# Optimization experiments

Hardware: AMD Instinct MI355X
Metric: run time of the kernel (lower is better)

Reference implementation:

```python
import jax, jax.numpy as jnp
from jax import lax
import numpy as np

B, IMG_H, IMG_W = 8, 256, 512
NUM_CLASSES, P = 20, 32
SCALE, TOPK, IOU_THR = 32.0, 100, 0.5


def conv2d(x, w, b, stride=1, pad=1):
    y = lax.conv_general_dilated(x, w, (stride, stride), [(pad, pad), (pad, pad)],
                                 dimension_numbers=('NCHW', 'OIHW', 'NCHW'))
    return y + b[None, :, None, None]


def bilinear_resize(img, out_h, out_w):
    # img: [..., H, W]; torch F.interpolate(mode='bilinear', align_corners=False)
    H, W = img.shape[-2], img.shape[-1]
    def idx_w(n_in, n_out):
        src = (jnp.arange(n_out, dtype=jnp.float32) + 0.5) * (n_in / n_out) - 0.5
        src = jnp.clip(src, 0.0, n_in - 1)
        i0 = jnp.floor(src).astype(jnp.int32)
        i1 = jnp.minimum(i0 + 1, n_in - 1)
        return i0, i1, src - i0.astype(jnp.float32)
    y0, y1, wy = idx_w(H, out_h)
    x0, x1, wx = idx_w(W, out_w)
    top = img[..., y0, :] * (1.0 - wy)[:, None] + img[..., y1, :] * wy[:, None]
    return top[..., x0] * (1.0 - wx) + top[..., x1] * wx


def generate_anchors(fh, fw):
    ys = (jnp.arange(fh, dtype=jnp.float32) + 0.5) * (IMG_H / fh)
    xs = (jnp.arange(fw, dtype=jnp.float32) + 0.5) * (IMG_W / fw)
    cy, cx = jnp.meshgrid(ys, xs, indexing='ij')
    h = SCALE / 2
    return jnp.stack([cx - h, cy - h, cx + h, cy + h], -1).reshape(-1, 4)


def delta_to_boxes(anchors, deltas):
    a_c = (anchors[:, :2] + anchors[:, 2:]) / 2
    a_wh = anchors[:, 2:] - anchors[:, :2]
    pc = a_c + deltas[..., :2] * a_wh
    pwh = a_wh * jnp.exp(deltas[..., 2:])
    return jnp.concatenate([pc - pwh / 2, pc + pwh / 2], -1)


def nms_single(boxes, scores, labels):
    # torchvision batched_nms: offset boxes per label, greedy NMS, return kept idxs
    N = boxes.shape[0]
    off = labels.astype(boxes.dtype) * (jnp.max(boxes) + 1.0)
    b = boxes + off[:, None]
    order = jnp.argsort(-scores)
    bs = b[order]
    area = (bs[:, 2] - bs[:, 0]) * (bs[:, 3] - bs[:, 1])
    lt = jnp.maximum(bs[:, None, :2], bs[None, :, :2])
    rb = jnp.minimum(bs[:, None, 2:], bs[None, :, 2:])
    wh = jnp.clip(rb - lt, 0.0)
    inter = wh[..., 0] * wh[..., 1]
    iou = inter / (area[:, None] + area[None, :] - inter + 1e-9)
    idxs = jnp.arange(N)
    def body(i, suppressed):
        keep_i = jnp.logical_not(suppressed[i])
        row = (iou[i] > IOU_THR) & (idxs > i)
        return jnp.where(keep_i, suppressed | row, suppressed)
    suppressed = lax.fori_loop(0, N, body, jnp.zeros(N, bool))
    keep_mask = ~suppressed
    rank = jnp.cumsum(keep_mask) - 1
    slots = jnp.where(keep_mask & (rank < TOPK), rank, TOPK)
    out = jnp.full(TOPK + 1, -1, jnp.int32).at[slots].set(order.astype(jnp.int32))
    return out[:TOPK]


def setup_inputs():
    key = jax.random.key(0)
    ks = jax.random.split(key, 17)
    def cw(k, o, i, kh, kw_):
        return jax.random.normal(k, (o, i, kh, kw_), jnp.float32) / np.sqrt(i * kh * kw_)
    return {
        'images': jax.random.normal(ks[0], (B, 3, IMG_H, IMG_W), jnp.float32),
        'w1': cw(ks[1], 64, 3, 3, 3),   'b1': jnp.zeros(64, jnp.float32),
        'w2': cw(ks[2], 128, 64, 3, 3), 'b2': jnp.zeros(128, jnp.float32),
        'w3': cw(ks[3], 256, 128, 3, 3),'b3': jnp.zeros(256, jnp.float32),
        'pw1': cw(ks[4], 256, 256, 3, 3), 'pb1': jnp.zeros(256, jnp.float32),
        'pw2': cw(ks[5], P, 256, 1, 1),   'pb2': jnp.zeros(P, jnp.float32),
        'cw_': cw(ks[6], NUM_CLASSES + 1, 256, 3, 3), 'cb': jnp.zeros(NUM_CLASSES + 1, jnp.float32),
        'bw': cw(ks[7], 4, 256, 3, 3),  'bb': jnp.zeros(4, jnp.float32),
        'kw': cw(ks[8], P, 256, 3, 3),  'kb': jnp.zeros(P, jnp.float32),
    }


def reference(images, w1, b1, w2, b2, w3, b3, pw1, pb1, pw2, pb2, cw_, cb, bw, bb, kw, kb):
    x = jax.nn.relu(conv2d(images, w1, b1, stride=2))
    x = jax.nn.relu(conv2d(x, w2, b2, stride=2))
    feat = jax.nn.relu(conv2d(x, w3, b3, stride=2))          # [B,256,32,64]
    proto = conv2d(jax.nn.relu(conv2d(feat, pw1, pb1)), pw2, pb2, pad=0)  # [B,P,32,64]
    fh, fw = feat.shape[2], feat.shape[3]
    def head(w, b, c):
        return conv2d(feat, w, b).transpose(0, 2, 3, 1).reshape(B, -1, c)
    cls = head(cw_, cb, NUM_CLASSES + 1)     # [B,N,C+1]
    box = head(bw, bb, 4)                    # [B,N,4]
    coef = head(kw, kb, P)                   # [B,N,P]
    anchors = generate_anchors(fh, fw)       # [N,4]
    probs = jax.nn.softmax(cls, -1)[..., :-1]
    scores = probs.max(-1)
    labels = probs.argmax(-1).astype(jnp.int32)
    boxes = delta_to_boxes(anchors, box)     # [B,N,4]
    keep = jax.vmap(nms_single)(boxes, scores, labels)   # [B,100], -1 pad
    valid = keep >= 0
    ki = jnp.clip(keep, 0)
    take = lambda a: jnp.take_along_axis(a, ki[..., None] if a.ndim == 3 else ki, axis=1)
    boxes_k = take(boxes) * valid[..., None]
    scores_k = take(scores) * valid
    labels_k = jnp.where(valid, take(labels), 0)
    coef_k = jnp.take_along_axis(coef, ki[..., None], axis=1)   # [B,100,P]
    m = jax.nn.sigmoid(jnp.einsum('bkp,bphw->bkhw', coef_k, proto))
    masks = bilinear_resize(m, IMG_H, IMG_W) > 0.5
    masks = masks & valid[..., None, None]
    return boxes_k, scores_k, labels_k, masks, valid
```

## Files before the change

kernel.cpp:

```cpp
#include <hip/hip_runtime.h>
#include <hip/hip_bf16.h>
#include <math.h>

#define BB 8
#define NCLS 21
#define NANCH 2048
#define TOPK_N 100

static const size_t OFF_X1HI = 0;
static const size_t OFF_X1LO = 34344960;
static const size_t OFF_X2HI = 68689920;
static const size_t OFF_X2LO = 86261760;
static const size_t OFF_FTHI = 103833600;
static const size_t OFF_FTLO = 113025024;
static const size_t ZERO_BYTES = 122216448;
static const size_t OFF_WT1  = 122216448;
static const size_t OFF_A2H  = 122223616;
static const size_t OFF_A2L  = 122371072;
static const size_t OFF_A3H  = 122518528;
static const size_t OFF_A3L  = 123108352;
static const size_t OFF_AHH  = 123698176;
static const size_t OFF_AHL  = 123993088;
static const size_t OFF_AP1H = 124288000;
static const size_t OFF_AP1L = 125467648;
static const size_t OFF_WTP2 = 126647296;
static const size_t OFF_BH   = 126680064;
static const size_t OFF_HOUT = 126680576;
static const size_t OFF_P1   = 130874880;
static const size_t OFF_PROTO= 147652096;
static const size_t OFF_BOXES= 149749248;
static const size_t OFF_SCORES=150011392;
static const size_t OFF_LABELS=150076928;
static const size_t OFF_ORDER= 150142464;
static const size_t OFF_SB   = 150208000;
static const size_t OFF_IOU  = 150470144;
static const size_t OFF_KEEP = 154664448;
static const size_t OFF_MAXB = 154668032;
static const size_t OFF_M    = 154668544;

static const size_t OUT_BOXES  = 0;
static const size_t OUT_SCORES = 3200;
static const size_t OUT_LABELS = 4000;
static const size_t OUT_MASKS  = 4800;
static const size_t OUT_VALID  = 104862400;

typedef __attribute__((ext_vector_type(8))) short bf16x8;
typedef __attribute__((ext_vector_type(4))) float f32x4;

__device__ __forceinline__ unsigned encf(float f){
  unsigned u = __float_as_uint(f);
  return (u & 0x80000000u) ? ~u : (u | 0x80000000u);
}
__device__ __forceinline__ float decf(unsigned u){
  unsigned b = (u & 0x80000000u) ? (u & 0x7fffffffu) : ~u;
  return __uint_as_float(b);
}
__device__ __forceinline__ short f2bf(float f){
  __hip_bfloat16 h = __float2bfloat16(f);
  return *(short*)&h;
}
__device__ __forceinline__ float bf2f(short h){
  return __uint_as_float(((unsigned)(unsigned short)h) << 16);
}

__global__ void initk(unsigned* maxb){
  if (threadIdx.x < BB) maxb[threadIdx.x] = 0u;
}

__global__ void zerok(float4* __restrict__ p, long n4){
  long i = (long)blockIdx.x*256 + threadIdx.x;
  if (i < n4) p[i] = make_float4(0.f,0.f,0.f,0.f);
}

template<int CIN,int COUT,int KK>
__global__ void packw(const float* __restrict__ w, float* __restrict__ wT){
  int i = blockIdx.x*256 + threadIdx.x;
  if (i >= CIN*KK*COUT) return;
  int co = i % COUT; int r = i / COUT;
  int ci = r / KK,  k = r % KK;
  wT[i] = w[(co*CIN + ci)*KK + k];
}

template<int CIN,int COUT>
__global__ void packA(const float* __restrict__ w, short* __restrict__ Ahi,
                      short* __restrict__ Alo){
  constexpr int K = CIN*9;
  constexpr int KS = K/32;
  int i = blockIdx.x*256 + threadIdx.x;
  if (i >= COUT*K) return;
  int sub  = i & 7;
  int lane = (i >> 3) & 63;
  int rest = i >> 9;
  int ks = rest % KS;
  int mt = rest / KS;
  int m = mt*16 + (lane & 15);
  int k = ks*32 + (lane >> 4)*8 + sub;
  int tap = k / CIN, ci = k - tap*CIN;
  float v = w[(m*CIN + ci)*9 + tap];
  short h = f2bf(v);
  Ahi[i] = h;
  Alo[i] = f2bf(v - bf2f(h));
}

__global__ void packAh(const float* __restrict__ cw, const float* __restrict__ bw,
                       const float* __restrict__ kw, const float* __restrict__ cb,
                       const float* __restrict__ bb, const float* __restrict__ kb,
                       short* __restrict__ Ahi, short* __restrict__ Alo,
                       float* __restrict__ bh){
  int i = blockIdx.x*256 + threadIdx.x;
  if (i < 64){
    float v = 0.f;
    if (i < 21) v = cb[i]; else if (i < 25) v = bb[i-21]; else if (i < 57) v = kb[i-25];
    bh[i] = v;
  }
  if (i >= 64*2304) return;
  constexpr int KS = 72;
  int sub  = i & 7;
  int lane = (i >> 3) & 63;
  int rest = i >> 9;
  int ks = rest % KS;
  int mt = rest / KS;
  int m = mt*16 + (lane & 15);
  int k = ks*32 + (lane >> 4)*8 + sub;
  int tap = k >> 8, ci = k & 255;
  float v = 0.f;
  if (m < 21)      v = cw[(m*256 + ci)*9 + tap];
  else if (m < 25) v = bw[((m-21)*256 + ci)*9 + tap];
  else if (m < 57) v = kw[((m-25)*256 + ci)*9 + tap];
  short h = f2bf(v);
  Ahi[i] = h;
  Alo[i] = f2bf(v - bf2f(h));
}

__global__ __launch_bounds__(256) void conv1k(const float* __restrict__ img,
    const float* __restrict__ wT, const float* __restrict__ bias,
    short* __restrict__ x1hi, short* __restrict__ x1lo){
  const int b   = blockIdx.z;
  const int co0 = blockIdx.y * 16;
  const int g   = blockIdx.x*256 + threadIdx.x;
  const int y  = g >> 7;
  const int x0 = (g & 127) << 1;

  float acc[16][2];
#pragma unroll
  for (int c=0;c<16;c++){
    float bv = bias[co0+c];
    acc[c][0] = bv; acc[c][1] = bv;
  }
  int   off[3][5];
  float msk[3][5];
#pragma unroll
  for (int kh=0;kh<3;kh++){
    int iy = y*2 - 1 + kh;
    bool okr = (iy >= 0) && (iy < 256);
    int ro = okr ? iy*512 : 0;
#pragma unroll
    for (int t=0;t<5;t++){
      int col = x0*2 - 1 + t;
      bool ok = okr && (col >= 0) && (col < 512);
      off[kh][t] = ok ? (ro + col) : 0;
      msk[kh][t] = ok ? 1.f : 0.f;
    }
  }
  const float* inb = img + (size_t)b*3*256*512;
  for (int ci=0; ci<3; ci++){
    const float* inc = inb + (size_t)ci*256*512;
    float v[3][5];
#pragma unroll
    for (int kh=0;kh<3;kh++)
#pragma unroll
      for (int t=0;t<5;t++)
        v[kh][t] = inc[off[kh][t]] * msk[kh][t];
    const float* wp = wT + ci*9*64 + co0;
#pragma unroll
    for (int kh=0;kh<3;kh++)
#pragma unroll
    for (int kw=0;kw<3;kw++){
      const float* wq = wp + (kh*3+kw)*64;
#pragma unroll
      for (int c=0;c<16;c++){
        float wv = wq[c];
        acc[c][0] = fmaf(wv, v[kh][2*0+kw], acc[c][0]);
        acc[c][1] = fmaf(wv, v[kh][2*1+kw], acc[c][1]);
      }
    }
  }
#pragma unroll
  for (int s=0;s<2;s++){
    short hv[16] __attribute__((aligned(16)));
    short lv[16] __attribute__((aligned(16)));
#pragma unroll
    for (int c=0;c<16;c++){
      float r = fmaxf(acc[c][s], 0.f);
      short h = f2bf(r);
      hv[c] = h;
      lv[c] = f2bf(r - bf2f(h));
    }
#pragma unroll
    for (int g2=0; g2<2; g2++){
      size_t ad = (((size_t)(b*8 + (co0>>3) + g2)*130 + (y+1))*258 + (x0+s+1))*8;
      *(bf16x8*)(x1hi + ad) = *(bf16x8*)(hv + g2*8);
      *(bf16x8*)(x1lo + ad) = *(bf16x8*)(lv + g2*8);
    }
  }
}

template<int CIN,int K,int M,int MW,int NW,int OW,int OHh,int S,int IPH,int IPW,
         bool SPLIT,int EMODE,int OPH,int OPW>
__global__ __launch_bounds__(NW*64) void cgemm(
    const short* __restrict__ Ahi, const short* __restrict__ Alo,
    const short* __restrict__ Bhi, const short* __restrict__ Blo,
    const float* __restrict__ bias, float* __restrict__ outf,
    short* __restrict__ outhi, short* __restrict__ outlo){
  static_assert(CIN % 32 == 0, "CIN must be multiple of 32");
  constexpr int NT = OW*OHh;
  constexpr int KS = K/32;
  constexpr int CG = CIN/8;
  const int b    = blockIdx.z;
  const int wave = threadIdx.x >> 6;
  const int lane = threadIdx.x & 63;
  const int lm = lane & 15, lq = lane >> 4;
  const int m0 = (blockIdx.y * NW + wave) * (MW*16);
  const int n0 = blockIdx.x * 64;

  int oy[4], ox[4];
#pragma unroll
  for (int j=0;j<4;j++){
    int n = n0 + j*16 + lm;
    oy[j] = n / OW; ox[j] = n % OW;
  }

  f32x4 acc[MW][4];
#pragma unroll
  for (int i=0;i<MW;i++)
#pragma unroll
    for (int j=0;j<4;j++) acc[i][j] = (f32x4){0.f,0.f,0.f,0.f};

  const short* Ah_l = Ahi + (size_t)lane*8;
  const short* Al_l = Alo + (size_t)lane*8;
  const int mt0 = m0 >> 4;

  const size_t plane = (size_t)IPH*IPW;
  const short* Bh0 = Bhi + ((size_t)b*CG + lq)*plane*8;
  const short* Bl0 = Blo + ((size_t)b*CG + lq)*plane*8;

#pragma unroll 3
  for (int tap=0; tap<9; tap++){
    const int dy = tap/3, dx = tap%3;
    size_t pix[4];
#pragma unroll
    for (int j=0;j<4;j++)
      pix[j] = (size_t)(oy[j]*S + dy)*IPW + (size_t)(ox[j]*S + dx);
    const int ksb = tap*(CIN/32);
#pragma unroll
    for (int kc=0; kc<CIN; kc+=32){
      const int ks = ksb + (kc>>5);
      const size_t koff = (size_t)(kc>>3)*plane;
      bf16x8 ah[MW], bh_[4];
#pragma unroll
      for (int i=0;i<MW;i++)
        ah[i] = *(const bf16x8*)(Ah_l + ((size_t)(mt0+i)*KS + ks)*512);
#pragma unroll
      for (int j=0;j<4;j++) bh_[j] = *(const bf16x8*)(Bh0 + (koff + pix[j])*8);
      if constexpr (SPLIT){
        bf16x8 al[MW], bl_[4];
#pragma unroll
        for (int i=0;i<MW;i++)
          al[i] = *(const bf16x8*)(Al_l + ((size_t)(mt0+i)*KS + ks)*512);
#pragma unroll
        for (int j=0;j<4;j++) bl_[j] = *(const bf16x8*)(Bl0 + (koff + pix[j])*8);
#pragma unroll
        for (int j=0;j<4;j++)
#pragma unroll
          for (int i=0;i<MW;i++)
            acc[i][j] = __builtin_amdgcn_mfma_f32_16x16x32_bf16(ah[i], bh_[j], acc[i][j], 0,0,0);
#pragma unroll
        for (int j=0;j<4;j++)
#pragma unroll
          for (int i=0;i<MW;i++)
            acc[i][j] = __builtin_amdgcn_mfma_f32_16x16x32_bf16(ah[i], bl_[j], acc[i][j], 0,0,0);
#pragma unroll
        for (int j=0;j<4;j++)
#pragma unroll
          for (int i=0;i<MW;i++)
            acc[i][j] = __builtin_amdgcn_mfma_f32_16x16x32_bf16(al[i], bh_[j], acc[i][j], 0,0,0);
      } else {
#pragma unroll
        for (int j=0;j<4;j++)
#pragma unroll
          for (int i=0;i<MW;i++)
            acc[i][j] = __builtin_amdgcn_mfma_f32_16x16x32_bf16(ah[i], bh_[j], acc[i][j], 0,0,0);
      }
    }
  }

#pragma unroll
  for (int i=0;i<MW;i++){
#pragma unroll
    for (int r=0;r<4;r++){
      const int m = m0 + i*16 + lq*4 + r;
      const float bv = bias[m];
      if constexpr (EMODE == 0){
#pragma unroll
        for (int j=0;j<4;j++){
          float v = fmaxf(acc[i][j][r] + bv, 0.f);
          short h = f2bf(v);
          short l = f2bf(v - bf2f(h));
          size_t ad = ((((size_t)(b*(M/8) + (m>>3))*OPH + (oy[j]+1))*OPW + (ox[j]+1)))*8 + (m&7);
          outhi[ad] = h;
          outlo[ad] = l;
        }
      } else {
        float* cp = outf + ((size_t)b*M + m)*NT + n0 + lm;
#pragma unroll
        for (int j=0;j<4;j++){
          float v = acc[i][j][r] + bv;
          if constexpr (EMODE == 2) v = fmaxf(v, 0.f);
          cp[j*16] = v;
        }
      }
    }
  }
}

__global__ __launch_bounds__(256) void pw2k2(const float* __restrict__ p1,
    const float* __restrict__ wT, const float* __restrict__ bias,
    float* __restrict__ proto){
  const int b  = blockIdx.y;
  const int sp = blockIdx.x*256 + threadIdx.x;
  float acc[32];
#pragma unroll
  for (int c=0;c<32;c++) acc[c] = bias[c];
  const float* pb = p1 + (size_t)b*256*NANCH + sp;
  for (int ci=0;ci<256;ci++){
    float v = pb[(size_t)ci*NANCH];
    const float* wq = wT + ci*32;
#pragma unroll
    for (int c=0;c<32;c++) acc[c] = fmaf(v, wq[c], acc[c]);
  }
#pragma unroll
  for (int c=0;c<32;c++)
    proto[((size_t)b*32 + c)*NANCH + sp] = acc[c];
}

__global__ void decodek(const float* __restrict__ hout,
                        float* __restrict__ boxes, float* __restrict__ scores,
                        int* __restrict__ labels, unsigned* __restrict__ maxb){
  const int b = blockIdx.y;
  const int n = blockIdx.x*blockDim.x + threadIdx.x;
  const float* cp = hout + (size_t)b*64*NANCH + n;
  float l[NCLS];
  float M = -1e30f;
#pragma unroll
  for (int c=0;c<NCLS;c++){ l[c] = cp[(size_t)c*NANCH]; M = fmaxf(M, l[c]); }
  float denom = 0.f;
#pragma unroll
  for (int c=0;c<NCLS;c++) denom += expf(l[c]-M);
  float best = -1.f; int bi = 0;
#pragma unroll
  for (int c=0;c<NCLS-1;c++){
    float e = expf(l[c]-M);
    if (e > best){ best = e; bi = c; }
  }
  scores[(size_t)b*NANCH + n] = best/denom;
  labels[(size_t)b*NANCH + n] = bi;

  float dx = cp[21*(size_t)NANCH], dy = cp[22*(size_t)NANCH];
  float dw = cp[23*(size_t)NANCH], dh = cp[24*(size_t)NANCH];
  const int yy = n >> 6, xx = n & 63;
  float cx = (xx+0.5f)*8.f, cy = (yy+0.5f)*8.f;
  float px = cx + dx*32.f, py = cy + dy*32.f;
  float pw = 32.f*expf(dw), ph = 32.f*expf(dh);
  float x1 = px - 0.5f*pw, y1 = py - 0.5f*ph;
  float x2 = px + 0.5f*pw, y2 = py + 0.5f*ph;
  float* bo = boxes + ((size_t)b*NANCH + n)*4;
  bo[0]=x1; bo[1]=y1; bo[2]=x2; bo[3]=y2;
  float mx = fmaxf(fmaxf(x1,y1), fmaxf(x2,y2));
#pragma unroll
  for (int off=32; off>0; off>>=1) mx = fmaxf(mx, __shfl_down(mx, off));
  if ((threadIdx.x & 63) == 0) atomicMax(maxb + b, encf(mx));
}

__global__ void __launch_bounds__(1024) sortk(const float* __restrict__ scores,
                     const float* __restrict__ boxes, const int* __restrict__ labels,
                     const unsigned* __restrict__ maxb,
                     int* __restrict__ order, float* __restrict__ sb){
  __shared__ float sc[NANCH];
  __shared__ int   id[NANCH];
  const int b = blockIdx.x, t = threadIdx.x;
  for (int i=t;i<NANCH;i+=1024){ sc[i]=scores[(size_t)b*NANCH+i]; id[i]=i; }
  __syncthreads();
  for (int k=2;k<=NANCH;k<<=1){
    for (int j=k>>1;j>0;j>>=1){
      for (int i=t;i<NANCH;i+=1024){
        int ixj = i ^ j;
        if (ixj > i){
          float sa=sc[i], sb_=sc[ixj]; int ia=id[i], ib=id[ixj];
          bool dir = ((i & k) == 0);
          bool before_ba = (sb_ > sa) || (sb_ == sa && ib < ia);
          if (before_ba == dir){ sc[i]=sb_; sc[ixj]=sa; id[i]=ib; id[ixj]=ia; }
        }
      }
      __syncthreads();
    }
  }
  float mboff = decf(maxb[b]) + 1.0f;
  for (int r=t;r<NANCH;r+=1024){
    int o = id[r];
    order[(size_t)b*NANCH + r] = o;
    float off = (float)labels[(size_t)b*NANCH + o] * mboff;
    const float* bo = boxes + ((size_t)b*NANCH + o)*4;
    float* sp = sb + ((size_t)b*NANCH + r)*4;
    sp[0]=bo[0]+off; sp[1]=bo[1]+off; sp[2]=bo[2]+off; sp[3]=bo[3]+off;
  }
}

__global__ void ioumask(const float* __restrict__ sb, unsigned long long* __restrict__ iou){
  const int b = blockIdx.y;
  const int gid = blockIdx.x*blockDim.x + threadIdx.x;
  const int i = gid >> 5, w = gid & 31;
  const float* base = sb + (size_t)b*NANCH*4;
  unsigned long long bits = 0ull;
  const int j0 = w << 6;
  if (j0 + 63 > i){
    float x1=base[i*4], y1=base[i*4+1], x2=base[i*4+2], y2=base[i*4+3];
    float ai = (x2-x1)*(y2-y1);
    for (int jj=0;jj<64;jj++){
      int j = j0 + jj;
      if (j > i){
        float bx1=base[j*4], by1=base[j*4+1], bx2=base[j*4+2], by2=base[j*4+3];
        float lx=fmaxf(x1,bx1), ly=fmaxf(y1,by1);
        float rx=fminf(x2,bx2), ry=fminf(y2,by2);
        float ww=fmaxf(rx-lx,0.f), hh=fmaxf(ry-ly,0.f);
        float inter = ww*hh;
        float aj = (bx2-bx1)*(by2-by1);
        float v = inter/(ai + aj - inter + 1e-9f);
        if (v > 0.5f) bits |= (1ull << jj);
      }
    }
  }
  iou[((size_t)b*NANCH + i)*32 + w] = bits;
}

__global__ void nmsscan(const unsigned long long* __restrict__ iou,
                        const int* __restrict__ order, int* __restrict__ keep){
  const int b = blockIdx.x, lane = threadIdx.x;
  unsigned long long sup = 0ull;
  int k = 0;
  for (int i=0; i<NANCH && k<TOPK_N; i++){
    int wi = i >> 6, bi = i & 63;
    unsigned long long wv = __shfl(sup, wi);
    if (!((wv >> bi) & 1ull)){
      if (lane == 0) keep[b*TOPK_N + k] = order[(size_t)b*NANCH + i];
      k++;
      unsigned long long row = (lane < 32) ? iou[((size_t)b*NANCH + i)*32 + lane] : 0ull;
      sup |= row;
    }
  }
  for (int r = lane; r < TOPK_N; r += 64)
    if (r >= k) keep[b*TOPK_N + r] = -1;
}

__global__ void gatherk(const int* __restrict__ keep, const float* __restrict__ boxes,
                        const float* __restrict__ scores, const int* __restrict__ labels,
                        float* __restrict__ out){
  const int b = blockIdx.x, r = threadIdx.x;
  if (r >= TOPK_N) return;
  int ki = keep[b*TOPK_N + r];
  float valid = (ki >= 0) ? 1.f : 0.f;
  int kc = (ki < 0) ? 0 : ki;
  const float* bo = boxes + ((size_t)b*NANCH + kc)*4;
#pragma unroll
  for (int c=0;c<4;c++) out[OUT_BOXES + ((size_t)b*TOPK_N + r)*4 + c] = bo[c]*valid;
  out[OUT_SCORES + b*TOPK_N + r] = scores[(size_t)b*NANCH + kc]*valid;
  out[OUT_LABELS + b*TOPK_N + r] = (ki >= 0) ? (float)labels[(size_t)b*NANCH + kc] : 0.f;
  out[OUT_VALID  + b*TOPK_N + r] = valid;
}

__global__ void maskm(const int* __restrict__ keep, const float* __restrict__ hout,
                      const float* __restrict__ proto, float* __restrict__ m){
  const int b = blockIdx.z, r = blockIdx.y;
  const int s = blockIdx.x*blockDim.x + threadIdx.x;
  __shared__ float cf[32];
  int ki = keep[b*TOPK_N + r];
  int kc = (ki < 0) ? 0 : ki;
  if (threadIdx.x < 32)
    cf[threadIdx.x] = hout[((size_t)b*64 + 25 + threadIdx.x)*NANCH + kc];
  __syncthreads();
  float acc = 0.f;
#pragma unroll
  for (int p=0;p<32;p++) acc = fmaf(cf[p], proto[((size_t)b*32 + p)*NANCH + s], acc);
  m[((size_t)b*TOPK_N + r)*NANCH + s] = 1.f/(1.f + expf(-acc));
}

__global__ void resizek(const float* __restrict__ m, const int* __restrict__ keep,
                        float* __restrict__ out){
  const int b = blockIdx.z, r = blockIdx.y;
  const int pid = blockIdx.x*blockDim.x + threadIdx.x;
  const int y  = pid >> 7;
  const int x4 = (pid & 127) << 2;
  bool valid = keep[b*TOPK_N + r] >= 0;
  const float* mb = m + ((size_t)b*TOPK_N + r)*NANCH;
  float sy = (y + 0.5f)*0.125f - 0.5f;
  sy = fminf(fmaxf(sy, 0.f), 31.f);
  int y0 = (int)floorf(sy);
  int y1 = min(y0+1, 31);
  float wy = sy - (float)y0;
  const float* r0 = mb + y0*64;
  const float* r1 = mb + y1*64;
  float res[4];
#pragma unroll
  for (int k=0;k<4;k++){
    int x = x4 + k;
    float sx = (x + 0.5f)*0.125f - 0.5f;
    sx = fminf(fmaxf(sx, 0.f), 63.f);
    int x0 = (int)floorf(sx);
    int x1 = min(x0+1, 63);
    float wx = sx - (float)x0;
    float t0 = r0[x0]*(1.f-wy) + r1[x0]*wy;
    float t1 = r0[x1]*(1.f-wy) + r1[x1]*wy;
    float v  = t0*(1.f-wx) + t1*wx;
    res[k] = (v > 0.5f && valid) ? 1.f : 0.f;
  }
  float4 v4 = make_float4(res[0], res[1], res[2], res[3]);
  *(float4*)(out + OUT_MASKS + (((size_t)b*TOPK_N + r)*256 + y)*512 + x4) = v4;
}

extern "C" void kernel_launch(void* const* d_in, const int* in_sizes, int n_in,
                              void* d_out, int out_size, void* d_ws, size_t ws_size,
                              hipStream_t stream) {
  const float* images=(const float*)d_in[0];
  const float* w1=(const float*)d_in[1];  const float* b1=(const float*)d_in[2];
  const float* w2=(const float*)d_in[3];  const float* b2=(const float*)d_in[4];
  const float* w3=(const float*)d_in[5];  const float* b3=(const float*)d_in[6];
  const float* pw1=(const float*)d_in[7]; const float* pb1=(const float*)d_in[8];
  const float* pw2=(const float*)d_in[9]; const float* pb2=(const float*)d_in[10];
  const float* cw=(const float*)d_in[11]; const float* cb=(const float*)d_in[12];
  const float* bw=(const float*)d_in[13]; const float* bb=(const float*)d_in[14];
  const float* kw=(const float*)d_in[15]; const float* kb=(const float*)d_in[16];
  float* out = (float*)d_out;
  char* ws = (char*)d_ws;

  short* x1hi = (short*)(ws + OFF_X1HI);
  short* x1lo = (short*)(ws + OFF_X1LO);
  short* x2hi = (short*)(ws + OFF_X2HI);
  short* x2lo = (short*)(ws + OFF_X2LO);
  short* fthi = (short*)(ws + OFF_FTHI);
  short* ftlo = (short*)(ws + OFF_FTLO);
  float* wT1  = (float*)(ws + OFF_WT1);
  short* a2h  = (short*)(ws + OFF_A2H);
  short* a2l  = (short*)(ws + OFF_A2L);
  short* a3h  = (short*)(ws + OFF_A3H);
  short* a3l  = (short*)(ws + OFF_A3L);
  short* ahh  = (short*)(ws + OFF_AHH);
  short* ahl  = (short*)(ws + OFF_AHL);
  short* ap1h = (short*)(ws + OFF_AP1H);
  short* ap1l = (short*)(ws + OFF_AP1L);
  float* wTp2 = (float*)(ws + OFF_WTP2);
  float* bh   = (float*)(ws + OFF_BH);
  float* hout = (float*)(ws + OFF_HOUT);
  float* p1   = (float*)(ws + OFF_P1);
  float* proto= (float*)(ws + OFF_PROTO);
  float* boxes= (float*)(ws + OFF_BOXES);
  float* scores=(float*)(ws + OFF_SCORES);
  int*   labels=(int*)  (ws + OFF_LABELS);
  int*   order =(int*)  (ws + OFF_ORDER);
  float* sb   = (float*)(ws + OFF_SB);
  unsigned long long* iou = (unsigned long long*)(ws + OFF_IOU);
  int*   keep = (int*)  (ws + OFF_KEEP);
  unsigned* maxb = (unsigned*)(ws + OFF_MAXB);
  float* m    = (float*)(ws + OFF_M);

  initk<<<dim3(1), dim3(64), 0, stream>>>(maxb);

  zerok<<<dim3((unsigned)(ZERO_BYTES/16/256)), 256, 0, stream>>>((float4*)ws, (long)(ZERO_BYTES/16));

  packw<3,64,9>  <<<dim3(7),    256, 0, stream>>>(w1, wT1);
  packA<64,128>  <<<dim3(288),  256, 0, stream>>>(w2, a2h, a2l);
  packA<128,256> <<<dim3(1152), 256, 0, stream>>>(w3, a3h, a3l);
  packA<256,256> <<<dim3(2304), 256, 0, stream>>>(pw1, ap1h, ap1l);
  packAh<<<dim3(576), 256, 0, stream>>>(cw, bw, kw, cb, bb, kb, ahh, ahl, bh);
  packw<256,32,1><<<dim3(32),   256, 0, stream>>>(pw2, wTp2);

  conv1k<<<dim3(64,4,BB), 256, 0, stream>>>(images, wT1, b1, x1hi, x1lo);

  cgemm<64,576,128,4,2,128,64,2,130,258,true,0,66,130>
      <<<dim3(128,1,BB), 128, 0, stream>>>(a2h, a2l, x1hi, x1lo, b2, nullptr, x2hi, x2lo);

  cgemm<128,1152,256,4,4,64,32,2,66,130,true,0,34,66>
      <<<dim3(32,1,BB), 256, 0, stream>>>(a3h, a3l, x2hi, x2lo, b3, nullptr, fthi, ftlo);

  cgemm<256,2304,64,2,2,64,32,1,34,66,true,1,1,1>
      <<<dim3(32,1,BB), 128, 0, stream>>>(ahh, ahl, fthi, ftlo, bh, hout, nullptr, nullptr);

  cgemm<256,2304,256,4,4,64,32,1,34,66,false,2,1,1>
      <<<dim3(32,1,BB), 256, 0, stream>>>(ap1h, ap1l, fthi, fthi, pb1, p1, nullptr, nullptr);

  pw2k2<<<dim3(8,BB), 256, 0, stream>>>(p1, wTp2, pb2, proto);

  decodek<<<dim3(8,BB), 256, 0, stream>>>(hout, boxes, scores, labels, maxb);
  sortk<<<dim3(BB), 1024, 0, stream>>>(scores, boxes, labels, maxb, order, sb);
  ioumask<<<dim3(256,BB), 256, 0, stream>>>(sb, iou);
  nmsscan<<<dim3(BB), 64, 0, stream>>>(iou, order, keep);
  gatherk<<<dim3(BB), 128, 0, stream>>>(keep, boxes, scores, labels, out);

  maskm<<<dim3(8,TOPK_N,BB), 256, 0, stream>>>(keep, hout, proto, m);
  resizek<<<dim3(128,TOPK_N,BB), 256, 0, stream>>>(m, keep, out);
}
```

Baseline: 1.017 ms.

## Replace bitonic sort with rank sort, retile conv GEMMs, fold maxb init

Replaces the single-block-per-image bitonic sort with a rank sort spread over 8 blocks per image, where each thread counts how many scores beat its own and scatters its index and offset box directly. Changes the cgemm warp tiling for several conv layers and adds a second grid dimension to split output channels, aiming for more parallelism across CUs. Folds the maxb init kernel into the zero kernel to save a launch. The rank sort does quadratic work per image, and the new GEMM template parameters must match the kernel's indexing over grid y.

```diff
diff --git a/kernel.cpp b/kernel.cpp
--- a/kernel.cpp
+++ b/kernel.cpp
@@ -63,12 +63,9 @@
   return __uint_as_float(((unsigned)(unsigned short)h) << 16);
 }
 
-__global__ void initk(unsigned* maxb){
-  if (threadIdx.x < BB) maxb[threadIdx.x] = 0u;
-}
-
-__global__ void zerok(float4* __restrict__ p, long n4){
+__global__ void zerok(float4* __restrict__ p, long n4, unsigned* __restrict__ maxb){
   long i = (long)blockIdx.x*256 + threadIdx.x;
+  if (i < BB) maxb[i] = 0u;
   if (i < n4) p[i] = make_float4(0.f,0.f,0.f,0.f);
 }
 
@@ -381,38 +378,29 @@
   if ((threadIdx.x & 63) == 0) atomicMax(maxb + b, encf(mx));
 }
 
-__global__ void __launch_bounds__(1024) sortk(const float* __restrict__ scores,
-                     const float* __restrict__ boxes, const int* __restrict__ labels,
-                     const unsigned* __restrict__ maxb,
-                     int* __restrict__ order, float* __restrict__ sb){
+__global__ __launch_bounds__(256) void ranksort(const float* __restrict__ scores,
+    const float* __restrict__ boxes, const int* __restrict__ labels,
+    const unsigned* __restrict__ maxb, int* __restrict__ order,
+    float* __restrict__ sb){
   __shared__ float sc[NANCH];
-  __shared__ int   id[NANCH];
-  const int b = blockIdx.x, t = threadIdx.x;
-  for (int i=t;i<NANCH;i+=1024){ sc[i]=scores[(size_t)b*NANCH+i]; id[i]=i; }
+  const int b = blockIdx.y;
+  const int i = blockIdx.x*256 + threadIdx.x;
+  for (int t = threadIdx.x; t < NANCH; t += 256)
+    sc[t] = scores[(size_t)b*NANCH + t];
   __syncthreads();
-  for (int k=2;k<=NANCH;k<<=1){
-    for (int j=k>>1;j>0;j>>=1){
-      for (int i=t;i<NANCH;i+=1024){
-        int ixj = i ^ j;
-        if (ixj > i){
-          float sa=sc[i], sb_=sc[ixj]; int ia=id[i], ib=id[ixj];
-          bool dir = ((i & k) == 0);
-          bool before_ba = (sb_ > sa) || (sb_ == sa && ib < ia);
-          if (before_ba == dir){ sc[i]=sb_; sc[ixj]=sa; id[i]=ib; id[ixj]=ia; }
-        }
-      }
-      __syncthreads();
-    }
-  }
+  const float si = sc[i];
+  int rank = 0;
+#pragma unroll 8
+  for (int j=0;j<NANCH;j++){
+    float sj = sc[j];
+    rank += (int)((sj > si) | ((sj == si) & (j < i)));
+  }
+  order[(size_t)b*NANCH + rank] = i;
   float mboff = decf(maxb[b]) + 1.0f;
-  for (int r=t;r<NANCH;r+=1024){
-    int o = id[r];
-    order[(size_t)b*NANCH + r] = o;
-    float off = (float)labels[(size_t)b*NANCH + o] * mboff;
-    const float* bo = boxes + ((size_t)b*NANCH + o)*4;
-    float* sp = sb + ((size_t)b*NANCH + r)*4;
-    sp[0]=bo[0]+off; sp[1]=bo[1]+off; sp[2]=bo[2]+off; sp[3]=bo[3]+off;
-  }
+  float off = (float)labels[(size_t)b*NANCH + i] * mboff;
+  const float* bo = boxes + ((size_t)b*NANCH + i)*4;
+  float* sp = sb + ((size_t)b*NANCH + rank)*4;
+  sp[0]=bo[0]+off; sp[1]=bo[1]+off; sp[2]=bo[2]+off; sp[3]=bo[3]+off;
 }
 
 __global__ void ioumask(const float* __restrict__ sb, unsigned long long* __restrict__ iou){
@@ -571,9 +559,7 @@
   unsigned* maxb = (unsigned*)(ws + OFF_MAXB);
   float* m    = (float*)(ws + OFF_M);
 
-  initk<<<dim3(1), dim3(64), 0, stream>>>(maxb);
-
-  zerok<<<dim3((unsigned)(ZERO_BYTES/16/256)), 256, 0, stream>>>((float4*)ws, (long)(ZERO_BYTES/16));
+  zerok<<<dim3((unsigned)(ZERO_BYTES/16/256)), 256, 0, stream>>>((float4*)ws, (long)(ZERO_BYTES/16), maxb);
 
   packw<3,64,9>  <<<dim3(7),    256, 0, stream>>>(w1, wT1);
   packA<64,128>  <<<dim3(288),  256, 0, stream>>>(w2, a2h, a2l);
@@ -584,22 +570,22 @@
 
   conv1k<<<dim3(64,4,BB), 256, 0, stream>>>(images, wT1, b1, x1hi, x1lo);
 
-  cgemm<64,576,128,4,2,128,64,2,130,258,true,0,66,130>
-      <<<dim3(128,1,BB), 128, 0, stream>>>(a2h, a2l, x1hi, x1lo, b2, nullptr, x2hi, x2lo);
-
-  cgemm<128,1152,256,4,4,64,32,2,66,130,true,0,34,66>
-      <<<dim3(32,1,BB), 256, 0, stream>>>(a3h, a3l, x2hi, x2lo, b3, nullptr, fthi, ftlo);
+  cgemm<64,576,128,2,4,128,64,2,130,258,true,0,66,130>
+      <<<dim3(128,1,BB), 256, 0, stream>>>(a2h, a2l, x1hi, x1lo, b2, nullptr, x2hi, x2lo);
+
+  cgemm<128,1152,256,2,4,64,32,2,66,130,true,0,34,66>
+      <<<dim3(32,2,BB), 256, 0, stream>>>(a3h, a3l, x2hi, x2lo, b3, nullptr, fthi, ftlo);
 
   cgemm<256,2304,64,2,2,64,32,1,34,66,true,1,1,1>
       <<<dim3(32,1,BB), 128, 0, stream>>>(ahh, ahl, fthi, ftlo, bh, hout, nullptr, nullptr);
 
-  cgemm<256,2304,256,4,4,64,32,1,34,66,false,2,1,1>
-      <<<dim3(32,1,BB), 256, 0, stream>>>(ap1h, ap1l, fthi, fthi, pb1, p1, nullptr, nullptr);
+  cgemm<256,2304,256,2,4,64,32,1,34,66,false,2,1,1>
+      <<<dim3(32,2,BB), 256, 0, stream>>>(ap1h, ap1l, fthi, fthi, pb1, p1, nullptr, nullptr);
 
   pw2k2<<<dim3(8,BB), 256, 0, stream>>>(p1, wTp2, pb2, proto);
 
   decodek<<<dim3(8,BB), 256, 0, stream>>>(hout, boxes, scores, labels, maxb);
-  sortk<<<dim3(BB), 1024, 0, stream>>>(scores, boxes, labels, maxb, order, sb);
+  ranksort<<<dim3(8,BB), 256, 0, stream>>>(scores, boxes, labels, maxb, order, sb);
   ioumask<<<dim3(256,BB), 256, 0, stream>>>(sb, iou);
   nmsscan<<<dim3(BB), 64, 0, stream>>>(iou, order, keep);
   gatherk<<<dim3(BB), 128, 0, stream>>>(keep, boxes, scores, labels, out);
```

Result: no change. 1.026 ms (+0.9%).
